# Performance work log

Measured on AMD Instinct MI355X. Metric: run time of the kernel, lower is better.

The kernel has to match this reference:

```python
import jax, jax.numpy as jnp
import numpy as np

B, L, H, E, D = 4, 2048, 8, 64, 64  # seq S == L (causal mask requires square scores)


def setup_inputs() -> dict:
    key = jax.random.key(0)
    k0, k1, k2, k3, k4 = jax.random.split(key, 5)
    queries = jax.random.normal(k0, (B, L, H, E), jnp.float32)
    keys = jax.random.normal(k1, (B, L, H, E), jnp.float32)
    values = jax.random.normal(k2, (B, L, H, D), jnp.float32)
    # per-sample learned de-stationary scale (positive) and bias
    tau = jax.random.uniform(k3, (B, 1, 1), jnp.float32, 0.5, 1.5)
    delta = jax.random.normal(k4, (B, 1, L), jnp.float32) * 0.1
    return {"queries": queries, "keys": keys, "values": values, "tau": tau, "delta": delta}


def reference(queries, keys, values, tau, delta):
    Bq, Lq, Hq, Eq = queries.shape
    S = keys.shape[1]
    scale = 1.0 / jnp.sqrt(jnp.asarray(Eq, jnp.float32))
    # torch path: rearrange('b s h d l -> (b d) s h l') with s=h=d=1 -> [B,1,1,1] / [B,1,1,S]
    tau_b = tau.reshape(Bq, 1, 1, 1)
    delta_b = delta.reshape(Bq, 1, 1, -1)[..., :S]
    # scores: [B, H, L, S]
    scores = jnp.einsum('blhe,bshe->bhls', queries, keys) * tau_b + delta_b
    causal = jnp.triu(jnp.ones((Lq, S), bool), k=1)  # True above diagonal -> masked
    scores = jnp.where(causal, -jnp.inf, scores)
    A = jax.nn.softmax(scale * scores, axis=-1)  # dropout is identity in eval/reference
    V = jnp.einsum('bhls,bshd->blhd', A, values)  # [B, L, H, D]
    return V
```

## Files before the change

### kernel.cpp

```cpp
#include <hip/hip_runtime.h>
#include <hip/hip_bf16.h>

#define Bsz 4
#define Lsz 2048
#define Hsz 8

typedef __attribute__((ext_vector_type(8)))  short bf16x8;
typedef __attribute__((ext_vector_type(4)))  short bf16x4;
typedef __attribute__((ext_vector_type(4)))  float f32x4;

__device__ __forceinline__ short f2bs(float f) {
    union { float f; unsigned u; } v; v.f = f;
    unsigned r = v.u + 0x7FFFu + ((v.u >> 16) & 1u);
    return (short)(r >> 16);
}
__device__ __forceinline__ short f2bs_rh(float f) {
    return (short)((__float_as_uint(f) + 0x8000u) >> 16);
}

__global__ __launch_bounds__(256, 3) void dsattn_fused(
    const float* __restrict__ q,
    const float* __restrict__ ksrc,
    const float* __restrict__ vsrc,
    const float* __restrict__ tau,
    const float* __restrict__ delta,
    float* __restrict__ out)
{
    __shared__ float dls[Lsz];
    __shared__ __align__(16) short Qs[4096];
    __shared__ __align__(16) float Ored[2][4096];

    const int tid  = threadIdx.x;
    const int kq   = tid >> 6;
    const int lane = tid & 63;
    const int ln   = lane & 15;
    const int quad = lane >> 4;

    const int bh = blockIdx.x;
    const int b  = bh >> 3, h = bh & 7;
    const int y = blockIdx.y, g8 = y >> 3, a = y & 7;
    const int qt = (g8 == 0) ? 31 - 2*a : (g8 == 1) ? 2*a
                 : (g8 == 2) ? 30 - 2*a : 2*a + 1;
    const int q0 = qt * 64;
    const int T  = qt + 1;

    const float c2  = 0.125f * 1.44269504f;
    const float st2 = c2 * tau[b];

    {
        const float* dsrc = delta + (size_t)b*Lsz + tid*8;
        float4 av = *(const float4*)(dsrc);
        float4 cv = *(const float4*)(dsrc + 4);
        av.x*=c2; av.y*=c2; av.z*=c2; av.w*=c2;
        cv.x*=c2; cv.y*=c2; cv.z*=c2; cv.w*=c2;
        *(float4*)&dls[tid*8]     = av;
        *(float4*)&dls[tid*8 + 4] = cv;
    }

    {
        const float* qrow = q + (((size_t)b*Lsz + q0 + kq*16 + ln)*Hsz + h)*64;
        float4 a0 = *(const float4*)(qrow + quad*8);
        float4 a1 = *(const float4*)(qrow + quad*8 + 4);
        float4 b0 = *(const float4*)(qrow + 32 + quad*8);
        float4 b1 = *(const float4*)(qrow + 32 + quad*8 + 4);
        bf16x8 q0f = {f2bs(a0.x),f2bs(a0.y),f2bs(a0.z),f2bs(a0.w),
                      f2bs(a1.x),f2bs(a1.y),f2bs(a1.z),f2bs(a1.w)};
        bf16x8 q1f = {f2bs(b0.x),f2bs(b0.y),f2bs(b0.z),f2bs(b0.w),
                      f2bs(b1.x),f2bs(b1.y),f2bs(b1.z),f2bs(b1.w)};
        *(bf16x8*)(&Qs[(kq*2+0)*512 + lane*8]) = q0f;
        *(bf16x8*)(&Qs[(kq*2+1)*512 + lane*8]) = q1f;
    }

    const float* kp = ksrc + (((size_t)b*Lsz + kq*16 + ln)*Hsz + h)*64 + quad*8;
    const float* vp = vsrc + (((size_t)b*Lsz + kq*16 + quad*4)*Hsz + h)*64 + ln;

    f32x4 oacc[4][4];
    #pragma unroll
    for (int dg = 0; dg < 4; ++dg)
        #pragma unroll
        for (int qg = 0; qg < 4; ++qg)
            oacc[dg][qg] = (f32x4){0.f,0.f,0.f,0.f};
    float l_acc[4] = {0.f,0.f,0.f,0.f};

    __syncthreads();

#define TILE_BODY(t_, MASKED) do {                                          \
        \
        const float4 ka0_ = *(const float4*)(kp);                           \
        const float4 ka1_ = *(const float4*)(kp + 4);                       \
        const float4 kb0_ = *(const float4*)(kp + 32);                      \
        const float4 kb1_ = *(const float4*)(kp + 36);                      \
        float vs_[16];                                                      \
        _Pragma("unroll")                                                   \
        for (int dg = 0; dg < 4; ++dg)                                      \
            _Pragma("unroll")                                               \
            for (int j = 0; j < 4; ++j)                                     \
                vs_[dg*4+j] = vp[j*512 + dg*16];                            \
          \
        bf16x8 kf0_ = {f2bs(ka0_.x),f2bs(ka0_.y),f2bs(ka0_.z),f2bs(ka0_.w),\
                       f2bs(ka1_.x),f2bs(ka1_.y),f2bs(ka1_.z),f2bs(ka1_.w)};\
        bf16x8 kf1_ = {f2bs(kb0_.x),f2bs(kb0_.y),f2bs(kb0_.z),f2bs(kb0_.w),\
                       f2bs(kb1_.x),f2bs(kb1_.y),f2bs(kb1_.z),f2bs(kb1_.w)};\
        f32x4 sacc_[4];                                                     \
        __builtin_amdgcn_s_setprio(1);                                      \
        _Pragma("unroll")                                                   \
        for (int qg = 0; qg < 4; ++qg) {                                    \
            bf16x8 qa_ = *(const bf16x8*)(&Qs[(qg*2+0)*512 + lane*8]);      \
            bf16x8 qb_ = *(const bf16x8*)(&Qs[(qg*2+1)*512 + lane*8]);      \
            f32x4 z_ = (f32x4){0.f,0.f,0.f,0.f};                            \
            z_ = __builtin_amdgcn_mfma_f32_16x16x32_bf16(kf0_, qa_, z_, 0,0,0); \
            sacc_[qg] = __builtin_amdgcn_mfma_f32_16x16x32_bf16(kf1_, qb_, z_, 0,0,0); \
        }                                                                   \
        __builtin_amdgcn_s_setprio(0);                                      \
        if (MASKED) {                                                       \
            _Pragma("unroll")                                               \
            for (int qg = 0; qg < 4; ++qg)                                  \
                _Pragma("unroll")                                           \
                for (int r = 0; r < 4; ++r)                                 \
                    if (kq*16 + quad*4 + r > qg*16 + ln) sacc_[qg][r] = -1e30f; \
        }                                                                   \
        f32x4 dlv_ = *(const f32x4*)&dls[(t_)*64 + kq*16 + quad*4];         \
        bf16x4 pT_[4];                                                      \
        _Pragma("unroll")                                                   \
        for (int qg = 0; qg < 4; ++qg) {                                    \
            float p0_ = __builtin_amdgcn_exp2f(fmaf(sacc_[qg][0], st2, dlv_[0])); \
            float p1_ = __builtin_amdgcn_exp2f(fmaf(sacc_[qg][1], st2, dlv_[1])); \
            float p2_ = __builtin_amdgcn_exp2f(fmaf(sacc_[qg][2], st2, dlv_[2])); \
            float p3_ = __builtin_amdgcn_exp2f(fmaf(sacc_[qg][3], st2, dlv_[3])); \
            l_acc[qg] += (p0_ + p1_) + (p2_ + p3_);                         \
            pT_[qg] = (bf16x4){f2bs_rh(p0_), f2bs_rh(p1_),                  \
                               f2bs_rh(p2_), f2bs_rh(p3_)};                 \
        }                                                                   \
                                \
        bf16x4 vf_[4];                                                      \
        _Pragma("unroll")                                                   \
        for (int dg = 0; dg < 4; ++dg)                                      \
            vf_[dg] = (bf16x4){f2bs(vs_[dg*4+0]), f2bs(vs_[dg*4+1]),        \
                               f2bs(vs_[dg*4+2]), f2bs(vs_[dg*4+3])};       \
        __builtin_amdgcn_s_setprio(1);                                      \
        _Pragma("unroll")                                                   \
        for (int dg = 0; dg < 4; ++dg)                                      \
            _Pragma("unroll")                                               \
            for (int qg = 0; qg < 4; ++qg)                                  \
                oacc[dg][qg] = __builtin_amdgcn_mfma_f32_16x16x16bf16_1k(   \
                    vf_[dg], pT_[qg], oacc[dg][qg], 0,0,0);                 \
        __builtin_amdgcn_s_setprio(0);                                      \
        kp += 32768; vp += 32768;                                           \
    } while (0)

    for (int t = 0; t < T - 1; ++t) TILE_BODY(t, false);
    TILE_BODY(T - 1, true);

    float lq[4];
    #pragma unroll
    for (int qg = 0; qg < 4; ++qg) {
        float s = l_acc[qg];
        s += __shfl_xor(s, 16, 64);
        s += __shfl_xor(s, 32, 64);
        lq[qg] = s;
    }
    float* KbF = &Ored[0][0];
    float* VbF = &Ored[1][0];
    float* lred = dls;
    __syncthreads();

    if (lane < 16)
        #pragma unroll
        for (int qg = 0; qg < 4; ++qg) lred[kq*64 + qg*16 + ln] = lq[qg];
    if (kq == 1 || kq == 3) {
        float* dst = (kq == 1) ? KbF : VbF;
        #pragma unroll
        for (int dg = 0; dg < 4; ++dg)
            #pragma unroll
            for (int qg = 0; qg < 4; ++qg)
                *(f32x4*)(dst + (dg*4+qg)*256 + lane*4) = oacc[dg][qg];
    }
    __syncthreads();
    if (kq == 0 || kq == 2) {
        const float* srcp = (kq == 0) ? KbF : VbF;
        #pragma unroll
        for (int dg = 0; dg < 4; ++dg)
            #pragma unroll
            for (int qg = 0; qg < 4; ++qg) {
                f32x4 v = *(const f32x4*)(srcp + (dg*4+qg)*256 + lane*4);
                oacc[dg][qg][0] += v[0]; oacc[dg][qg][1] += v[1];
                oacc[dg][qg][2] += v[2]; oacc[dg][qg][3] += v[3];
            }
    }
    __syncthreads();
    if (kq == 2) {
        #pragma unroll
        for (int dg = 0; dg < 4; ++dg)
            #pragma unroll
            for (int qg = 0; qg < 4; ++qg)
                *(f32x4*)(KbF + (dg*4+qg)*256 + lane*4) = oacc[dg][qg];
    }
    __syncthreads();
    if (kq == 0) {
        float inv[4];
        #pragma unroll
        for (int qg = 0; qg < 4; ++qg)
            inv[qg] = 1.0f / (lred[qg*16 + ln] + lred[64 + qg*16 + ln]
                            + lred[128 + qg*16 + ln] + lred[192 + qg*16 + ln]);
        #pragma unroll
        for (int qg = 0; qg < 4; ++qg) {
            float* orow = out + (((size_t)b*Lsz + q0 + qg*16 + ln)*Hsz + h)*64;
            #pragma unroll
            for (int dg = 0; dg < 4; ++dg) {
                f32x4 v = *(const f32x4*)(KbF + (dg*4+qg)*256 + lane*4);
                float4 o = {(oacc[dg][qg][0] + v[0]) * inv[qg],
                            (oacc[dg][qg][1] + v[1]) * inv[qg],
                            (oacc[dg][qg][2] + v[2]) * inv[qg],
                            (oacc[dg][qg][3] + v[3]) * inv[qg]};
                *(float4*)(orow + dg*16 + quad*4) = o;
            }
        }
    }
#undef TILE_BODY
}

extern "C" void kernel_launch(void* const* d_in, const int* in_sizes, int n_in,
                              void* d_out, int out_size, void* d_ws, size_t ws_size,
                              hipStream_t stream) {
    (void)in_sizes; (void)n_in; (void)out_size; (void)d_ws; (void)ws_size;
    const float* q     = (const float*)d_in[0];
    const float* k     = (const float*)d_in[1];
    const float* v     = (const float*)d_in[2];
    const float* tau   = (const float*)d_in[3];
    const float* delta = (const float*)d_in[4];
    float* out = (float*)d_out;

    dsattn_fused<<<dim3(Bsz*Hsz, 32), dim3(256), 0, stream>>>(q, k, v, tau, delta, out);
}
```

Baseline: 138.9 us.

## Double-buffer K/V register loads and simplify tile scheduling order

Prefetches the next K/V tile's global loads into a second register set while the current tile's MFMAs and exp run, ping-ponging between buffers A and B with a 2x unrolled loop. The aim is to hide global memory latency behind compute. It also replaces the interleaved heavy/light query-tile ordering with a plain descending order (heaviest first). This raises register pressure, which could reduce occupancy under launch_bounds(256,3) or cause spills.

```diff
diff --git a/kernel.cpp b/kernel.cpp
--- a/kernel.cpp
+++ b/kernel.cpp
@@ -38,9 +38,7 @@
 
     const int bh = blockIdx.x;
     const int b  = bh >> 3, h = bh & 7;
-    const int y = blockIdx.y, g8 = y >> 3, a = y & 7;
-    const int qt = (g8 == 0) ? 31 - 2*a : (g8 == 1) ? 2*a
-                 : (g8 == 2) ? 30 - 2*a : 2*a + 1;
+    const int qt = 31 - blockIdx.y;
     const int q0 = qt * 64;
     const int T  = qt + 1;
 
@@ -82,25 +80,37 @@
             oacc[dg][qg] = (f32x4){0.f,0.f,0.f,0.f};
     float l_acc[4] = {0.f,0.f,0.f,0.f};
 
-    __syncthreads();
-
-#define TILE_BODY(t_, MASKED) do {                                          \
-        \
-        const float4 ka0_ = *(const float4*)(kp);                           \
-        const float4 ka1_ = *(const float4*)(kp + 4);                       \
-        const float4 kb0_ = *(const float4*)(kp + 32);                      \
-        const float4 kb1_ = *(const float4*)(kp + 36);                      \
-        float vs_[16];                                                      \
-        _Pragma("unroll")                                                   \
-        for (int dg = 0; dg < 4; ++dg)                                      \
+    float4 Aka0, Aka1, Akb0, Akb1; float Avs[16];
+    float4 Bka0, Bka1, Bkb0, Bkb1; float Bvs[16];
+
+    Aka0 = *(const float4*)(kp);      Aka1 = *(const float4*)(kp + 4);
+    Akb0 = *(const float4*)(kp + 32); Akb1 = *(const float4*)(kp + 36);
+    #pragma unroll
+    for (int dg = 0; dg < 4; ++dg)
+        #pragma unroll
+        for (int j = 0; j < 4; ++j)
+            Avs[dg*4+j] = vp[j*512 + dg*16];
+
+    __syncthreads();
+
+#define TILE_BODY(t_, MASKED, HASNEXT, C, N) do {                           \
+        if (HASNEXT) {                                                      \
+            kp += 32768; vp += 32768;                                       \
+            N##ka0 = *(const float4*)(kp);                                  \
+            N##ka1 = *(const float4*)(kp + 4);                              \
+            N##kb0 = *(const float4*)(kp + 32);                             \
+            N##kb1 = *(const float4*)(kp + 36);                             \
             _Pragma("unroll")                                               \
-            for (int j = 0; j < 4; ++j)                                     \
-                vs_[dg*4+j] = vp[j*512 + dg*16];                            \
-          \
-        bf16x8 kf0_ = {f2bs(ka0_.x),f2bs(ka0_.y),f2bs(ka0_.z),f2bs(ka0_.w),\
-                       f2bs(ka1_.x),f2bs(ka1_.y),f2bs(ka1_.z),f2bs(ka1_.w)};\
-        bf16x8 kf1_ = {f2bs(kb0_.x),f2bs(kb0_.y),f2bs(kb0_.z),f2bs(kb0_.w),\
-                       f2bs(kb1_.x),f2bs(kb1_.y),f2bs(kb1_.z),f2bs(kb1_.w)};\
+            for (int dg = 0; dg < 4; ++dg)                                  \
+                _Pragma("unroll")                                           \
+                for (int j = 0; j < 4; ++j)                                 \
+                    N##vs[dg*4+j] = vp[j*512 + dg*16];                      \
+        }                                                                   \
+              \
+        bf16x8 kf0_ = {f2bs(C##ka0.x),f2bs(C##ka0.y),f2bs(C##ka0.z),f2bs(C##ka0.w), \
+                       f2bs(C##ka1.x),f2bs(C##ka1.y),f2bs(C##ka1.z),f2bs(C##ka1.w)}; \
+        bf16x8 kf1_ = {f2bs(C##kb0.x),f2bs(C##kb0.y),f2bs(C##kb0.z),f2bs(C##kb0.w), \
+                       f2bs(C##kb1.x),f2bs(C##kb1.y),f2bs(C##kb1.z),f2bs(C##kb1.w)}; \
         f32x4 sacc_[4];                                                     \
         __builtin_amdgcn_s_setprio(1);                                      \
         _Pragma("unroll")                                                   \
@@ -135,8 +145,8 @@
         bf16x4 vf_[4];                                                      \
         _Pragma("unroll")                                                   \
         for (int dg = 0; dg < 4; ++dg)                                      \
-            vf_[dg] = (bf16x4){f2bs(vs_[dg*4+0]), f2bs(vs_[dg*4+1]),        \
-                               f2bs(vs_[dg*4+2]), f2bs(vs_[dg*4+3])};       \
+            vf_[dg] = (bf16x4){f2bs(C##vs[dg*4+0]), f2bs(C##vs[dg*4+1]),    \
+                               f2bs(C##vs[dg*4+2]), f2bs(C##vs[dg*4+3])};   \
         __builtin_amdgcn_s_setprio(1);                                      \
         _Pragma("unroll")                                                   \
         for (int dg = 0; dg < 4; ++dg)                                      \
@@ -145,11 +155,19 @@
                 oacc[dg][qg] = __builtin_amdgcn_mfma_f32_16x16x16bf16_1k(   \
                     vf_[dg], pT_[qg], oacc[dg][qg], 0,0,0);                 \
         __builtin_amdgcn_s_setprio(0);                                      \
-        kp += 32768; vp += 32768;                                           \
     } while (0)
 
-    for (int t = 0; t < T - 1; ++t) TILE_BODY(t, false);
-    TILE_BODY(T - 1, true);
+    int t = 0;
+    for (; t + 2 <= T - 1; t += 2) {
+        TILE_BODY(t,     false, true, A, B);
+        TILE_BODY(t + 1, false, true, B, A);
+    }
+    if (t < T - 1) {
+        TILE_BODY(t, false, true, A, B);
+        TILE_BODY(T - 1, true, false, B, A);
+    } else {
+        TILE_BODY(T - 1, true, false, A, B);
+    }
 
     float lq[4];
     #pragma unroll
```

Result: slower. 357.1 us (+157.0%).
